# Optimization experiments

Measured on AMD Instinct MI355X. Metric: run time of the kernel, lower is better.

Reference implementation:

```python
import jax, jax.numpy as jnp
import numpy as np

V, E = 50000, 300        # vocab, word2vec embedding dim
B, T = 64, 512           # batch, sequence length
U1, U2, DD = 64, 32, 32  # brnn1 units, brnn2 units, dense units


def _glorot(k, shape):
    lim = np.sqrt(6.0 / (shape[0] + shape[1])).astype(np.float32)
    return jax.random.uniform(k, shape, jnp.float32, -lim, lim)


def setup_inputs() -> dict:
    key = jax.random.key(0)
    ks = jax.random.split(key, 12)
    return {
        "token_ids": jax.random.randint(ks[0], (B, T), 0, V),
        "emb": jax.random.normal(ks[1], (V, E), jnp.float32) * 0.05,
        # per-cell gate weights stacked [f|i|c|o] along output dim (same math as 4 separate matmuls)
        "w1f": _glorot(ks[2], (E + U1, 4 * U1)), "b1f": jnp.zeros((4 * U1,), jnp.float32),
        "w1b": _glorot(ks[3], (E + U1, 4 * U1)), "b1b": jnp.zeros((4 * U1,), jnp.float32),
        "w2f": _glorot(ks[4], (2 * U1 + U2, 4 * U2)), "b2f": jnp.zeros((4 * U2,), jnp.float32),
        "w2b": _glorot(ks[5], (2 * U1 + U2, 4 * U2)), "b2b": jnp.zeros((4 * U2,), jnp.float32),
        "wd": _glorot(ks[6], (2 * U2, DD)), "bd": jnp.zeros((DD,), jnp.float32),
        "wo": _glorot(ks[7], (DD, 1)), "bo": jnp.zeros((1,), jnp.float32),
    }


def _lstm(xs, W, b, units, reverse=False):
    # xs: (T, B, D). Single fused gate matmul per step; scan carries (h, c).
    h0 = jnp.zeros((xs.shape[1], units), xs.dtype)
    c0 = jnp.zeros_like(h0)

    def step(carry, x_t):
        h, c = carry
        z = jnp.concatenate([x_t, h], axis=-1) @ W + b  # (B, 4U)
        f, i, g, o = jnp.split(z, 4, axis=-1)
        f = jax.nn.sigmoid(f)
        i = jax.nn.sigmoid(i)
        g = jnp.tanh(g)
        o = jax.nn.sigmoid(o)
        c_new = f * c + i * g
        h_new = o * jnp.tanh(c_new)
        return (h_new, c_new), h_new

    (hT, _), ys = jax.lax.scan(step, (h0, c0), xs, reverse=reverse)
    return ys, hT  # ys: (T, B, U) in original time order; hT = final hidden


def reference(token_ids, emb, w1f, b1f, w1b, b1b, w2f, b2f, w2b, b2b, wd, bd, wo, bo):
    x = emb[token_ids]                      # (B, T, E) frozen word2vec lookup
    xs = jnp.transpose(x, (1, 0, 2))        # (T, B, E)
    # BRNN layer 1: return_sequences=True, merge='concat'
    yf, _ = _lstm(xs, w1f, b1f, U1)
    yb, _ = _lstm(xs, w1b, b1b, U1, reverse=True)
    h1 = jnp.concatenate([yf, yb], axis=-1)  # (T, B, 2*U1); dropout1 = identity at inference
    # BRNN layer 2: return_sequences=False -> final fwd h and final bwd h, concat
    _, hf = _lstm(h1, w2f, b2f, U2)
    _, hb = _lstm(h1, w2b, b2b, U2, reverse=True)
    h2 = jnp.concatenate([hf, hb], axis=-1)  # (B, 2*U2)
    d = jax.nn.relu(h2 @ wd + bd)            # dense head; dropout2 = identity
    return jax.nn.sigmoid(d @ wo + bo)       # (B, 1) sentiment probability
```

## Files before the change

kernel.cpp:

```cpp
#include <hip/hip_runtime.h>

#define T_LEN 512

typedef _Float16 h2_t  __attribute__((ext_vector_type(2)));
typedef _Float16 f16x8 __attribute__((ext_vector_type(8)));
typedef float    f32x4 __attribute__((ext_vector_type(4)));

__device__ __forceinline__ float sigf(float x) {
    return 1.0f / (1.0f + __expf(-x));
}
__device__ __forceinline__ float tanhf_(float x) {
    return 2.0f / (1.0f + __expf(-2.0f * x)) - 1.0f;
}
__device__ __forceinline__ unsigned pack2(float x, float y) {
    h2_t p; p[0] = (_Float16)x; p[1] = (_Float16)y;
    return __builtin_bit_cast(unsigned, p);
}
__device__ __forceinline__ h2_t d2u(unsigned x) {
    return __builtin_bit_cast(h2_t, x);
}

__device__ __forceinline__ float dpp_xor1(float x) {
    int i = __builtin_bit_cast(int, x);
    i = __builtin_amdgcn_mov_dpp(i, 0xB1, 0xF, 0xF, true);
    return __builtin_bit_cast(float, i);
}
__device__ __forceinline__ float dpp_xor2(float x) {
    int i = __builtin_bit_cast(int, x);
    i = __builtin_amdgcn_mov_dpp(i, 0x4E, 0xF, 0xF, true);
    return __builtin_bit_cast(float, i);
}

#if defined(__has_builtin)
#  if __has_builtin(__builtin_amdgcn_fdot2)
#    define FDOT2(a, b, c) __builtin_amdgcn_fdot2((a), (b), (c), false)
#  endif
#endif
#ifndef FDOT2
__device__ __forceinline__ float fdot2_fb(h2_t a, h2_t b, float c) {
    return fmaf((float)a[0], (float)b[0], fmaf((float)a[1], (float)b[1], c));
}
#  define FDOT2(a, b, c) fdot2_fb((a), (b), (c))
#endif

__device__ __forceinline__ void lds_barrier() {
    asm volatile("s_waitcnt lgkmcnt(0)" ::: "memory");
    __builtin_amdgcn_s_barrier();
    asm volatile("" ::: "memory");
}

__global__ __launch_bounds__(64) void prep_w1(
    const float* __restrict__ w1f, const float* __restrict__ w1b,
    _Float16* __restrict__ Wt1)
{
    const int col = blockIdx.x;
    const int t   = threadIdx.x;
    if (t >= 40) return;
    const float* __restrict__ W = (col < 256) ? w1f : w1b;
    const int c = col & 255;
    f16x8 v;
    #pragma unroll
    for (int i = 0; i < 8; ++i) {
        int k = t * 8 + i;
        float x = (k < 300) ? W[(size_t)k * 256 + c] : 0.0f;
        v[i] = (_Float16)x;
    }
    *(f16x8*)(Wt1 + (size_t)col * 320 + t * 8) = v;
}

__global__ __launch_bounds__(64) void prep_w2(
    const float* __restrict__ w2f, const float* __restrict__ w2b,
    _Float16* __restrict__ Wt2)
{
    const int col = blockIdx.x;
    const int t   = threadIdx.x;
    if (t >= 16) return;
    const float* __restrict__ W = (col < 128) ? w2f : w2b;
    const int c = col & 127;
    f16x8 v;
    #pragma unroll
    for (int i = 0; i < 8; ++i) {
        int k = t * 8 + i;
        v[i] = (_Float16)W[(size_t)k * 128 + c];
    }
    *(f16x8*)(Wt2 + (size_t)col * 128 + t * 8) = v;
}

__global__ __launch_bounds__(64) void prep_whr1(
    const float* __restrict__ w1f, const float* __restrict__ w1b,
    _Float16* __restrict__ Whr1)
{
    const int x    = blockIdx.x;
    const int dir  = x >> 8, colp = x & 255;
    const int u = colp >> 2, g = colp & 3;
    const int k = threadIdx.x;
    const float* __restrict__ W = dir ? w1b : w1f;
    Whr1[(size_t)x * 64 + k] = (_Float16)W[(size_t)(300 + k) * 256 + g * 64 + u];
}

__global__ __launch_bounds__(64) void prep_whr2(
    const float* __restrict__ w2f, const float* __restrict__ w2b,
    _Float16* __restrict__ Whr2)
{
    const int x    = blockIdx.x;
    const int dir  = x >> 7, colp = x & 127;
    const int u = colp >> 2, g = colp & 3;
    const int k = threadIdx.x;
    if (k >= 32) return;
    const float* __restrict__ W = dir ? w2b : w2f;
    Whr2[(size_t)x * 32 + k] = (_Float16)W[(size_t)(128 + k) * 128 + g * 32 + u];
}

__global__ __launch_bounds__(256, 1) void gemm1_kernel(
    const int* __restrict__ tok, const float* __restrict__ emb,
    const _Float16* __restrict__ Wt1,
    const float* __restrict__ b1f, const float* __restrict__ b1b,
    float* __restrict__ Z1)
{
    const int row0 = blockIdx.x * 64;
    const int b    = row0 >> 9;
    const int t0   = row0 & 511;
    const int tid  = threadIdx.x;

    __shared__ __align__(16) _Float16 A_lds[64][328];

    {
        const int row = tid >> 2, q = tid & 3;
        const int tk = tok[b * T_LEN + t0 + row];
        const float* __restrict__ src = emb + (size_t)tk * 300 + q * 80;
        #pragma unroll
        for (int i = 0; i < 20; ++i) {
            float4 v;
            if (q == 3 && i >= 15) v = make_float4(0.f, 0.f, 0.f, 0.f);
            else                   v = *(const float4*)(src + i * 4);
            uint2 u; u.x = pack2(v.x, v.y); u.y = pack2(v.z, v.w);
            *(uint2*)&A_lds[row][q * 80 + i * 4] = u;
        }
    }
    __syncthreads();

    const int l   = tid & 63;
    const int w   = tid >> 6;
    const int wN0 = w * 128;
    const int lr  = l & 15;
    const int lk8 = (l >> 4) * 8;

    f32x4 acc[4][8] = {};

    #pragma unroll 2
    for (int ks = 0; ks < 10; ++ks) {
        const int k0 = ks * 32;
        f16x8 af[4];
        #pragma unroll
        for (int m = 0; m < 4; ++m)
            af[m] = *(const f16x8*)&A_lds[m * 16 + lr][k0 + lk8];
        f16x8 bf[8];
        #pragma unroll
        for (int n = 0; n < 8; ++n)
            bf[n] = *(const f16x8*)(Wt1 + (size_t)(wN0 + n * 16 + lr) * 320 + k0 + lk8);
        #pragma unroll
        for (int m = 0; m < 4; ++m)
            #pragma unroll
            for (int n = 0; n < 8; ++n)
                acc[m][n] = __builtin_amdgcn_mfma_f32_16x16x32_f16(af[m], bf[n], acc[m][n], 0, 0, 0);
    }

    const int dir = wN0 >> 8;
    const int rq  = (l >> 4) * 4;
    #pragma unroll
    for (int n = 0; n < 8; ++n) {
        const int colr = (wN0 + n * 16 + lr) & 255;
        const float bv = dir ? b1b[colr] : b1f[colr];
        #pragma unroll
        for (int m = 0; m < 4; ++m) {
            const size_t rb = (size_t)dir * 32768 + row0 + m * 16 + rq;
            #pragma unroll
            for (int r = 0; r < 4; ++r)
                Z1[(rb + r) * 256 + colr] = acc[m][n][r] + bv;
        }
    }
}

__global__ __launch_bounds__(256, 1) void gemm2_kernel(
    const _Float16* __restrict__ H1f,
    const _Float16* __restrict__ Wt2,
    const float* __restrict__ b2f, const float* __restrict__ b2b,
    float* __restrict__ Z2p)
{
    const int row0 = blockIdx.x * 64;
    const int tid  = threadIdx.x;

    __shared__ __align__(16) _Float16 A_lds[64][136];

    {
        const int row = tid >> 2, q = tid & 3;
        const _Float16* __restrict__ src = H1f + (size_t)(row0 + row) * 128 + q * 32;
        #pragma unroll
        for (int i = 0; i < 4; ++i)
            *(f16x8*)&A_lds[row][q * 32 + i * 8] = *(const f16x8*)(src + i * 8);
    }
    __syncthreads();

    const int l   = tid & 63;
    const int w   = tid >> 6;
    const int wN0 = w * 64;
    const int lr  = l & 15;
    const int lk8 = (l >> 4) * 8;

    f32x4 acc[4][4] = {};

    #pragma unroll
    for (int ks = 0; ks < 4; ++ks) {
        const int k0 = ks * 32;
        f16x8 af[4];
        #pragma unroll
        for (int m = 0; m < 4; ++m)
            af[m] = *(const f16x8*)&A_lds[m * 16 + lr][k0 + lk8];
        f16x8 bf[4];
        #pragma unroll
        for (int n = 0; n < 4; ++n)
            bf[n] = *(const f16x8*)(Wt2 + (size_t)(wN0 + n * 16 + lr) * 128 + k0 + lk8);
        #pragma unroll
        for (int m = 0; m < 4; ++m)
            #pragma unroll
            for (int n = 0; n < 4; ++n)
                acc[m][n] = __builtin_amdgcn_mfma_f32_16x16x32_f16(af[m], bf[n], acc[m][n], 0, 0, 0);
    }

    const int dir = wN0 >> 7;
    const int rq  = (l >> 4) * 4;
    #pragma unroll
    for (int n = 0; n < 4; ++n) {
        const int colr = (wN0 + n * 16 + lr) & 127;
        const int colp = (colr & 31) * 4 + (colr >> 5);
        const float bv = dir ? b2b[colr] : b2f[colr];
        #pragma unroll
        for (int m = 0; m < 4; ++m) {
            const size_t rb = (size_t)dir * 32768 + row0 + m * 16 + rq;
            #pragma unroll
            for (int r = 0; r < 4; ++r)
                Z2p[(rb + r) * 128 + colp] = acc[m][n][r] + bv;
        }
    }
}

__global__ __launch_bounds__(256, 1) void lstm1_kernel(
    const float* __restrict__ Z1,
    const _Float16* __restrict__ Whr1,
    _Float16* __restrict__ H1f)
{
    const int b   = blockIdx.x & 63;
    const int dir = blockIdx.x >> 6;
    const int tid = threadIdx.x;
    const int w   = tid >> 6;
    const int l   = tid & 63;
    const int g   = l & 3;
    const int u   = w * 16 + (l >> 2);
    const int col = g * 64 + u;

    h2_t wc[32];
    {
        const _Float16* __restrict__ wp = Whr1 + (size_t)(dir * 256 + w * 64 + l) * 64;
        #pragma unroll
        for (int r8 = 0; r8 < 8; ++r8) {
            f16x8 v = *(const f16x8*)(wp + r8 * 8);
            #pragma unroll
            for (int j = 0; j < 4; ++j) {
                h2_t p; p[0] = v[2 * j]; p[1] = v[2 * j + 1];
                wc[r8 * 4 + j] = p;
            }
        }
    }

    __shared__ __align__(16) _Float16 hbuf[2][64];
    if (tid < 64) { hbuf[0][tid] = (_Float16)0.0f; hbuf[1][tid] = (_Float16)0.0f; }
    lds_barrier();

    float c = 0.0f;

    const float* __restrict__ zcol =
        Z1 + ((size_t)(dir * 64 + b) * T_LEN) * 256 + col;

    float zr[4];
    #pragma unroll
    for (int q = 0; q < 4; ++q) {
        int t = dir ? (T_LEN - 1 - q) : q;
        zr[q] = zcol[(size_t)t * 256];
    }

    _Float16* __restrict__ hout = H1f + (size_t)b * T_LEN * 128 + dir * 64 + u;

    const bool s0b = (g & 1) != 0, s1b = (g >> 1) != 0;
    const float km  = (g == 2) ? -2.0f : -1.0f;
    const float num = (g == 2) ?  2.0f :  1.0f;
    const float off = (g == 2) ?  1.0f :  0.0f;

    for (int sb = 0; sb < T_LEN; sb += 4) {
        #pragma unroll
        for (int q = 0; q < 4; ++q) {
            const int s = sb + q;
            const uint4* hb = (const uint4*)hbuf[s & 1];
            float a0 = zr[q], a1 = 0.f, a2 = 0.f, a3 = 0.f;
            #pragma unroll
            for (int k = 0; k < 8; ++k) {
                uint4 hq = hb[k];
                h2_t p0 = __builtin_bit_cast(h2_t, hq.x);
                h2_t p1 = __builtin_bit_cast(h2_t, hq.y);
                h2_t p2 = __builtin_bit_cast(h2_t, hq.z);
                h2_t p3 = __builtin_bit_cast(h2_t, hq.w);
                a0 = FDOT2(p0, wc[4 * k + 0], a0);
                a1 = FDOT2(p1, wc[4 * k + 1], a1);
                a2 = FDOT2(p2, wc[4 * k + 2], a2);
                a3 = FDOT2(p3, wc[4 * k + 3], a3);
            }
            float zz = (a0 + a1) + (a2 + a3);

            {
                int sp = s + 4; if (sp > T_LEN - 1) sp = T_LEN - 1;
                int tp = dir ? (T_LEN - 1 - sp) : sp;
                zr[q] = zcol[(size_t)tp * 256];
            }

            float e = __expf(km * zz);
            float A = num / (1.0f + e) - off;
            float B = dpp_xor1(A);
            float C = dpp_xor2(A);
            float D = dpp_xor2(B);
            float f_ = s1b ? (s0b ? D : C) : (s0b ? B : A);
            float i_ = s1b ? (s0b ? C : D) : (s0b ? A : B);
            float g_ = s1b ? (s0b ? B : A) : (s0b ? D : C);
            float o_ = s1b ? (s0b ? A : B) : (s0b ? C : D);
            c = fmaf(f_, c, i_ * g_);
            float h = o_ * tanhf_(c);
            _Float16 h16 = (_Float16)h;
            if (g == 0) {
                int t = dir ? (T_LEN - 1 - s) : s;
                hout[(size_t)t * 128] = h16;
                hbuf[(s + 1) & 1][u] = h16;
            }
            lds_barrier();
        }
    }
}

__global__ __launch_bounds__(64, 1) void lstm2_kernel(
    const float* __restrict__ Z2p,
    const _Float16* __restrict__ Whr2,
    float* __restrict__ H2)
{
    const int b   = blockIdx.x & 63;
    const int dir = blockIdx.x >> 6;
    const int l   = threadIdx.x;
    const int p   = l & 1;
    const int u   = l >> 1;

    const uint4* __restrict__ wp0 =
        (const uint4*)(Whr2 + (size_t)(dir * 128 + u * 4 + p) * 32);
    const uint4* __restrict__ wp1 =
        (const uint4*)(Whr2 + (size_t)(dir * 128 + u * 4 + p + 2) * 32);
    const uint4 W00 = wp0[0], W01 = wp0[1], W02 = wp0[2], W03 = wp0[3];
    const uint4 W10 = wp1[0], W11 = wp1[1], W12 = wp1[2], W13 = wp1[3];

    __shared__ __align__(16) _Float16 hbuf[32];
    if (p == 0) hbuf[u] = (_Float16)0.0f;
    lds_barrier();

    float c = 0.0f, h = 0.0f;

    const float* __restrict__ zrow =
        Z2p + ((size_t)(dir * 64 + b) * T_LEN) * 128 + u * 4;

    float4 zA, zB, zC, zD;
    { int t = dir ? (T_LEN - 1) : 0; zA = *(const float4*)(zrow + (size_t)t * 128); }
    { int t = dir ? (T_LEN - 2) : 1; zB = *(const float4*)(zrow + (size_t)t * 128); }
    { int t = dir ? (T_LEN - 3) : 2; zC = *(const float4*)(zrow + (size_t)t * 128); }
    { int t = dir ? (T_LEN - 4) : 3; zD = *(const float4*)(zrow + (size_t)t * 128); }

    const float km  = (p == 0) ? -2.0f : -1.0f;
    const float num = (p == 0) ?  2.0f :  1.0f;
    const float off = (p == 0) ?  1.0f :  0.0f;

    const uint4* __restrict__ hb = (const uint4*)hbuf;

#define KBLK(HQ, WA, WB)                              \
    a00 = FDOT2(d2u(HQ.x), d2u(WA.x), a00);           \
    a01 = FDOT2(d2u(HQ.y), d2u(WA.y), a01);           \
    a00 = FDOT2(d2u(HQ.z), d2u(WA.z), a00);           \
    a01 = FDOT2(d2u(HQ.w), d2u(WA.w), a01);           \
    a10 = FDOT2(d2u(HQ.x), d2u(WB.x), a10);           \
    a11 = FDOT2(d2u(HQ.y), d2u(WB.y), a11);           \
    a10 = FDOT2(d2u(HQ.z), d2u(WB.z), a10);           \
    a11 = FDOT2(d2u(HQ.w), d2u(WB.w), a11);

#define L2_STEP(ZREG, QOFF)                                               \
    {                                                                     \
        const int s = sb + (QOFF);                                        \
        float zc0 = p ? ZREG.y : ZREG.x;                                  \
        float zc1 = p ? ZREG.w : ZREG.z;                                  \
        uint4 h0 = hb[0], h1 = hb[1], h2q = hb[2], h3 = hb[3];            \
        float a00 = zc0, a01 = 0.f, a10 = zc1, a11 = 0.f;                 \
        KBLK(h0, W00, W10)                                                \
        KBLK(h1, W01, W11)                                                \
        KBLK(h2q, W02, W12)                                               \
        KBLK(h3, W03, W13)                                                \
        float z0s = a00 + a01;                                            \
        float z1s = a10 + a11;                                            \
        {           \
            int sp = s + 4; if (sp > T_LEN - 1) sp = T_LEN - 1;           \
            int tp = dir ? (T_LEN - 1 - sp) : sp;                         \
            ZREG = *(const float4*)(zrow + (size_t)tp * 128);             \
        }                                                                 \
        float act0 = sigf(z0s);                   \
        float e = __expf(km * z1s);                                       \
        float act1 = num / (1.0f + e) - off;      \
        float x0 = dpp_xor1(act0);                                        \
        float x1 = dpp_xor1(act1);                                        \
        float f_ = p ? x0   : act0;                                       \
        float i_ = p ? act0 : x0;                                         \
        float g_ = p ? x1   : act1;                                       \
        float o_ = p ? act1 : x1;                                         \
        c = fmaf(f_, c, i_ * g_);                                         \
        h = o_ * tanhf_(c);                                               \
        if (p == 0) hbuf[u] = (_Float16)h;             \
        lds_barrier();                            \
    }

    for (int sb = 0; sb < T_LEN; sb += 4) {
        L2_STEP(zA, 0)
        L2_STEP(zB, 1)
        L2_STEP(zC, 2)
        L2_STEP(zD, 3)
    }
#undef L2_STEP
#undef KBLK

    if (p == 0)
        H2[(size_t)b * 64 + dir * 32 + u] = h;
}

__global__ __launch_bounds__(256) void head_kernel(
    const float* __restrict__ H2,
    const float* __restrict__ wd, const float* __restrict__ bd,
    const float* __restrict__ wo, const float* __restrict__ bo,
    float* __restrict__ out)
{
    const int tid = threadIdx.x;
    const int b = tid >> 2, qd = tid & 3;

    float hv[64];
    #pragma unroll
    for (int v = 0; v < 64; ++v) hv[v] = H2[b * 64 + v];

    float part = 0.0f;
    #pragma unroll
    for (int iq = 0; iq < 8; ++iq) {
        int i = qd * 8 + iq;
        float a = bd[i];
        #pragma unroll
        for (int v = 0; v < 64; ++v)
            a = fmaf(hv[v], wd[v * 32 + i], a);
        a = fmaxf(a, 0.0f);
        part = fmaf(a, wo[i], part);
    }

    __shared__ float ps[256];
    ps[tid] = part;
    __syncthreads();
    if (qd == 0) {
        float s = ps[tid] + ps[tid + 1] + ps[tid + 2] + ps[tid + 3];
        out[b] = sigf(s + bo[0]);
    }
}

extern "C" void kernel_launch(void* const* d_in, const int* in_sizes, int n_in,
                              void* d_out, int out_size, void* d_ws, size_t ws_size,
                              hipStream_t stream)
{
    const int*   tok = (const int*)  d_in[0];
    const float* emb = (const float*)d_in[1];
    const float* w1f = (const float*)d_in[2];
    const float* b1f = (const float*)d_in[3];
    const float* w1b = (const float*)d_in[4];
    const float* b1b = (const float*)d_in[5];
    const float* w2f = (const float*)d_in[6];
    const float* b2f = (const float*)d_in[7];
    const float* w2b = (const float*)d_in[8];
    const float* b2b = (const float*)d_in[9];
    const float* wd  = (const float*)d_in[10];
    const float* bd  = (const float*)d_in[11];
    const float* wo  = (const float*)d_in[12];
    const float* bo  = (const float*)d_in[13];
    float* out = (float*)d_out;

    float*    Z1   = (float*)d_ws;
    _Float16* H1f  = (_Float16*)(Z1 + (size_t)16777216);
    float*    H2   = (float*)(H1f + (size_t)4194304);
    _Float16* Wt1  = (_Float16*)(H2 + 4096);
    _Float16* Wt2  = Wt1 + (size_t)512 * 320;
    _Float16* Whr1 = Wt2 + (size_t)256 * 128;
    _Float16* Whr2 = Whr1 + (size_t)512 * 64;
    float*    Z2p  = Z1;

    prep_w1  <<<512, 64, 0, stream>>>(w1f, w1b, Wt1);
    prep_w2  <<<256, 64, 0, stream>>>(w2f, w2b, Wt2);
    prep_whr1<<<512, 64, 0, stream>>>(w1f, w1b, Whr1);
    prep_whr2<<<256, 64, 0, stream>>>(w2f, w2b, Whr2);
    gemm1_kernel<<<512, 256, 0, stream>>>(tok, emb, Wt1, b1f, b1b, Z1);
    lstm1_kernel<<<128, 256, 0, stream>>>(Z1, Whr1, H1f);
    gemm2_kernel<<<512, 256, 0, stream>>>(H1f, Wt2, b2f, b2b, Z2p);
    lstm2_kernel<<<128, 64, 0, stream>>>(Z2p, Whr2, H2);
    head_kernel<<<1, 256, 0, stream>>>(H2, wd, bd, wo, bo, out);
}
```

Before: 378.2 us.

## Compute two gate columns per thread in lstm1 with 128-thread blocks

Restructures the layer-1 recurrent kernel so each thread computes two gate pre-activations (a pair of columns) instead of one, halving the block size from 256 to 128 threads (two waves instead of four). The gate exchange now needs only one DPP xor1 swap per activation instead of xor1/xor2 combinations, and the recurrent weights are held as 16 uint4 registers per thread. The goal is to shorten the per-timestep barrier cost and cross-lane shuffling on the serial critical path. In exchange each thread does twice the dot-product work per step and uses more registers.

```diff
diff --git a/kernel.cpp b/kernel.cpp
--- a/kernel.cpp
+++ b/kernel.cpp
@@ -49,6 +49,16 @@
     asm volatile("" ::: "memory");
 }
 
+#define GACC(P, HQA, HQB, WA, WB)                     \
+    P = FDOT2(d2u(HQA.x), d2u(WA.x), P);              \
+    P = FDOT2(d2u(HQA.y), d2u(WA.y), P);              \
+    P = FDOT2(d2u(HQA.z), d2u(WA.z), P);              \
+    P = FDOT2(d2u(HQA.w), d2u(WA.w), P);              \
+    P = FDOT2(d2u(HQB.x), d2u(WB.x), P);              \
+    P = FDOT2(d2u(HQB.y), d2u(WB.y), P);              \
+    P = FDOT2(d2u(HQB.z), d2u(WB.z), P);              \
+    P = FDOT2(d2u(HQB.w), d2u(WB.w), P);
+
 __global__ __launch_bounds__(64) void prep_w1(
     const float* __restrict__ w1f, const float* __restrict__ w1b,
     _Float16* __restrict__ Wt1)
@@ -244,7 +254,7 @@
     }
 }
 
-__global__ __launch_bounds__(256, 1) void lstm1_kernel(
+__global__ __launch_bounds__(128, 1) void lstm1_kernel(
     const float* __restrict__ Z1,
     const _Float16* __restrict__ Whr1,
     _Float16* __restrict__ H1f)
@@ -254,23 +264,17 @@
     const int tid = threadIdx.x;
     const int w   = tid >> 6;
     const int l   = tid & 63;
-    const int g   = l & 3;
-    const int u   = w * 16 + (l >> 2);
-    const int col = g * 64 + u;
-
-    h2_t wc[32];
-    {
-        const _Float16* __restrict__ wp = Whr1 + (size_t)(dir * 256 + w * 64 + l) * 64;
-        #pragma unroll
-        for (int r8 = 0; r8 < 8; ++r8) {
-            f16x8 v = *(const f16x8*)(wp + r8 * 8);
-            #pragma unroll
-            for (int j = 0; j < 4; ++j) {
-                h2_t p; p[0] = v[2 * j]; p[1] = v[2 * j + 1];
-                wc[r8 * 4 + j] = p;
-            }
-        }
-    }
+    const int p   = l & 1;
+    const int u   = w * 32 + (l >> 1);
+
+    const uint4* __restrict__ w0p =
+        (const uint4*)(Whr1 + (size_t)(dir * 256 + u * 4 + p) * 64);
+    const uint4* __restrict__ w1p =
+        (const uint4*)(Whr1 + (size_t)(dir * 256 + u * 4 + p + 2) * 64);
+    const uint4 W00 = w0p[0], W01 = w0p[1], W02 = w0p[2], W03 = w0p[3];
+    const uint4 W04 = w0p[4], W05 = w0p[5], W06 = w0p[6], W07 = w0p[7];
+    const uint4 W10 = w1p[0], W11 = w1p[1], W12 = w1p[2], W13 = w1p[3];
+    const uint4 W14 = w1p[4], W15 = w1p[5], W16 = w1p[6], W17 = w1p[7];
 
     __shared__ __align__(16) _Float16 hbuf[2][64];
     if (tid < 64) { hbuf[0][tid] = (_Float16)0.0f; hbuf[1][tid] = (_Float16)0.0f; }
@@ -278,69 +282,72 @@
 
     float c = 0.0f;
 
-    const float* __restrict__ zcol =
-        Z1 + ((size_t)(dir * 64 + b) * T_LEN) * 256 + col;
-
-    float zr[4];
-    #pragma unroll
-    for (int q = 0; q < 4; ++q) {
-        int t = dir ? (T_LEN - 1 - q) : q;
-        zr[q] = zcol[(size_t)t * 256];
-    }
+    const float* __restrict__ zc0 =
+        Z1 + ((size_t)(dir * 64 + b) * T_LEN) * 256 + p * 64 + u;
+    const float* __restrict__ zc1 = zc0 + 128;
+
+    float zA0, zB0, zC0, zD0, zA1, zB1, zC1, zD1;
+    { int t = dir ? 511 : 0; zA0 = zc0[(size_t)t * 256]; zA1 = zc1[(size_t)t * 256]; }
+    { int t = dir ? 510 : 1; zB0 = zc0[(size_t)t * 256]; zB1 = zc1[(size_t)t * 256]; }
+    { int t = dir ? 509 : 2; zC0 = zc0[(size_t)t * 256]; zC1 = zc1[(size_t)t * 256]; }
+    { int t = dir ? 508 : 3; zD0 = zc0[(size_t)t * 256]; zD1 = zc1[(size_t)t * 256]; }
 
     _Float16* __restrict__ hout = H1f + (size_t)b * T_LEN * 128 + dir * 64 + u;
 
-    const bool s0b = (g & 1) != 0, s1b = (g >> 1) != 0;
-    const float km  = (g == 2) ? -2.0f : -1.0f;
-    const float num = (g == 2) ?  2.0f :  1.0f;
-    const float off = (g == 2) ?  1.0f :  0.0f;
+    const float km  = (p == 0) ? -2.0f : -1.0f;
+    const float num = (p == 0) ?  2.0f :  1.0f;
+    const float off = (p == 0) ?  1.0f :  0.0f;
+
+#define STEP1(ZR0V, ZR1V, QOFF)                                             \
+    {                                                                       \
+        const int s = sb + (QOFF);                                          \
+        const uint4* hb = (const uint4*)hbuf[s & 1];                        \
+        uint4 H0 = hb[0], H1v = hb[1], H2v = hb[2], H3v = hb[3];            \
+        uint4 H4v = hb[4], H5v = hb[5], H6v = hb[6], H7v = hb[7];           \
+        float a00 = ZR0V, a01 = 0.f, a10 = ZR1V, a11 = 0.f;                 \
+        GACC(a00, H0, H1v, W00, W01)                                        \
+        GACC(a01, H2v, H3v, W02, W03)                                       \
+        GACC(a10, H0, H1v, W10, W11)                                        \
+        GACC(a11, H2v, H3v, W12, W13)                                       \
+        GACC(a00, H4v, H5v, W04, W05)                                       \
+        GACC(a01, H6v, H7v, W06, W07)                                       \
+        GACC(a10, H4v, H5v, W14, W15)                                       \
+        GACC(a11, H6v, H7v, W16, W17)                                       \
+        float z0s = a00 + a01;                                              \
+        float z1s = a10 + a11;                                              \
+        {           \
+            int sp = s + 4; if (sp > 511) sp = 511;                         \
+            int tp = dir ? (511 - sp) : sp;                                 \
+            ZR0V = zc0[(size_t)tp * 256];                                   \
+            ZR1V = zc1[(size_t)tp * 256];                                   \
+        }                                                                   \
+        float act0 = sigf(z0s);                     \
+        float e = __expf(km * z1s);                                         \
+        float act1 = num / (1.0f + e) - off;        \
+        float x0 = dpp_xor1(act0);                                          \
+        float x1 = dpp_xor1(act1);                                          \
+        float f_ = p ? x0   : act0;                                         \
+        float i_ = p ? act0 : x0;                                           \
+        float g_ = p ? x1   : act1;                                         \
+        float o_ = p ? act1 : x1;                                           \
+        c = fmaf(f_, c, i_ * g_);                                           \
+        float h = o_ * tanhf_(c);                                           \
+        if (p == 0) {                                                       \
+            int t = dir ? (511 - s) : s;                                    \
+            _Float16 h16 = (_Float16)h;                                     \
+            hout[(size_t)t * 128] = h16;                                    \
+            hbuf[(s + 1) & 1][u] = h16;                                     \
+        }                                                                   \
+        lds_barrier();                                                      \
+    }
 
     for (int sb = 0; sb < T_LEN; sb += 4) {
-        #pragma unroll
-        for (int q = 0; q < 4; ++q) {
-            const int s = sb + q;
-            const uint4* hb = (const uint4*)hbuf[s & 1];
-            float a0 = zr[q], a1 = 0.f, a2 = 0.f, a3 = 0.f;
-            #pragma unroll
-            for (int k = 0; k < 8; ++k) {
-                uint4 hq = hb[k];
-                h2_t p0 = __builtin_bit_cast(h2_t, hq.x);
-                h2_t p1 = __builtin_bit_cast(h2_t, hq.y);
-                h2_t p2 = __builtin_bit_cast(h2_t, hq.z);
-                h2_t p3 = __builtin_bit_cast(h2_t, hq.w);
-                a0 = FDOT2(p0, wc[4 * k + 0], a0);
-                a1 = FDOT2(p1, wc[4 * k + 1], a1);
-                a2 = FDOT2(p2, wc[4 * k + 2], a2);
-                a3 = FDOT2(p3, wc[4 * k + 3], a3);
-            }
-            float zz = (a0 + a1) + (a2 + a3);
-
-            {
-                int sp = s + 4; if (sp > T_LEN - 1) sp = T_LEN - 1;
-                int tp = dir ? (T_LEN - 1 - sp) : sp;
-                zr[q] = zcol[(size_t)tp * 256];
-            }
-
-            float e = __expf(km * zz);
-            float A = num / (1.0f + e) - off;
-            float B = dpp_xor1(A);
-            float C = dpp_xor2(A);
-            float D = dpp_xor2(B);
-            float f_ = s1b ? (s0b ? D : C) : (s0b ? B : A);
-            float i_ = s1b ? (s0b ? C : D) : (s0b ? A : B);
-            float g_ = s1b ? (s0b ? B : A) : (s0b ? D : C);
-            float o_ = s1b ? (s0b ? A : B) : (s0b ? C : D);
-            c = fmaf(f_, c, i_ * g_);
-            float h = o_ * tanhf_(c);
-            _Float16 h16 = (_Float16)h;
-            if (g == 0) {
-                int t = dir ? (T_LEN - 1 - s) : s;
-                hout[(size_t)t * 128] = h16;
-                hbuf[(s + 1) & 1][u] = h16;
-            }
-            lds_barrier();
-        }
-    }
+        STEP1(zA0, zA1, 0)
+        STEP1(zB0, zB1, 1)
+        STEP1(zC0, zC1, 2)
+        STEP1(zD0, zD1, 3)
+    }
+#undef STEP1
 }
 
 __global__ __launch_bounds__(64, 1) void lstm2_kernel(
@@ -506,7 +513,7 @@
     prep_whr1<<<512, 64, 0, stream>>>(w1f, w1b, Whr1);
     prep_whr2<<<256, 64, 0, stream>>>(w2f, w2b, Whr2);
     gemm1_kernel<<<512, 256, 0, stream>>>(tok, emb, Wt1, b1f, b1b, Z1);
-    lstm1_kernel<<<128, 256, 0, stream>>>(Z1, Whr1, H1f);
+    lstm1_kernel<<<128, 128, 0, stream>>>(Z1, Whr1, H1f);
     gemm2_kernel<<<512, 256, 0, stream>>>(H1f, Wt2, b2f, b2b, Z2p);
     lstm2_kernel<<<128, 64, 0, stream>>>(Z2p, Whr2, H2);
     head_kernel<<<1, 256, 0, stream>>>(H2, wd, bd, wo, bo, out);
```

Result: slower. 408.6 us (+8.0%).
